# Kernel optimization log

Measured on AMD Instinct MI355X. Metric: run time of the kernel, lower is better.

The kernel has to match this reference:

```python
import jax, jax.numpy as jnp
import numpy as np

B, S, XDIM, YDIM = 64, 1024, 256, 128


def setup_inputs() -> dict:
    key = jax.random.key(0)
    ks = jax.random.split(key, 7)
    q = jax.random.normal(ks[0], (B, S, XDIM), dtype=jnp.float32)
    # Linear weights in torch layout [out, in]; biases [out]
    sc = 1.0 / np.sqrt(XDIM)
    Wq = jax.random.normal(ks[1], (YDIM, XDIM), dtype=jnp.float32) * sc
    Wk = jax.random.normal(ks[2], (YDIM, XDIM), dtype=jnp.float32) * sc
    Wv = jax.random.normal(ks[3], (YDIM, XDIM), dtype=jnp.float32) * sc
    bq = jax.random.normal(ks[4], (YDIM,), dtype=jnp.float32) * sc
    bk = jax.random.normal(ks[5], (YDIM,), dtype=jnp.float32) * sc
    bv = jax.random.normal(ks[6], (YDIM,), dtype=jnp.float32) * sc
    return {"q": q, "Wq": Wq, "bq": bq, "Wk": Wk, "bk": bk, "Wv": Wv, "bv": bv}


def reference(q, Wq, bq, Wk, bk, Wv, bv):
    # Q, K, V projections: [B, S, YDIM]
    Q = jnp.einsum('bsx,yx->bsy', q, Wq) + bq
    K = jnp.einsum('bsx,yx->bsy', q, Wk) + bk
    V = jnp.einsum('bsx,yx->bsy', q, Wv) + bv
    scale = jnp.float32(np.sqrt(YDIM))
    # scores [B, S_q, S_k]; softmax over the QUERY axis (dim=-2), non-standard
    scores = jnp.einsum('bqd,bkd->bqk', Q, K) / scale
    attn = jax.nn.softmax(scores, axis=-2)
    out = jnp.einsum('bqk,bkd->bqd', attn, V)  # [B, S, YDIM]
    # flat=True: max over dim=-2 -> [B, YDIM]
    return jnp.max(out, axis=-2)
```

## Files before the change

kernel.cpp:

```cpp
#include <hip/hip_runtime.h>

typedef __bf16 bf16;
typedef __attribute__((ext_vector_type(8))) __bf16 bf16x8;
typedef __attribute__((ext_vector_type(4))) __bf16 bf16x4;
typedef __attribute__((ext_vector_type(4))) float  f32x4;

static __device__ __forceinline__ f32x4 mfma16(bf16x8 a, bf16x8 b, f32x4 c) {
  return __builtin_amdgcn_mfma_f32_16x16x32_bf16(a, b, c, 0, 0, 0);
}
static __device__ __forceinline__ float fexp2(float x) {
  return __builtin_amdgcn_exp2f(x);
}
static __device__ __forceinline__ float flog2(float x) {
  return __builtin_amdgcn_logf(x);
}

#define EXP_C1 (1.4426950408889634f / 11.313708498984760f)

typedef const __attribute__((address_space(1))) unsigned int gas_u32;
typedef __attribute__((address_space(3))) unsigned int las_u32;
#define GLDS16(gp, lp) __builtin_amdgcn_global_load_lds((gas_u32*)(gp), (las_u32*)(lp), 16, 0, 0)

#define DMA_FENCE() __asm__ volatile("s_waitcnt vmcnt(0)" ::: "memory")


__global__ __launch_bounds__(256) void k_prep(
    const float* __restrict__ Wq, const float* __restrict__ Wk,
    const float* __restrict__ Wv, bf16* __restrict__ Wc, float* __restrict__ out)
{
  int id = blockIdx.x * 256 + threadIdx.x;
  if (id < 8192) out[id] = -__builtin_inff();
  int proj = id >> 12, r = id & 4095;
  int g = r >> 7, n = r & 127;
  const float* W = proj == 0 ? Wq : proj == 1 ? Wk : Wv;
  const float sc = (proj == 0) ? EXP_C1 : 1.0f;
  const float4* src = (const float4*)(W + n * 256 + g * 8);
  float4 a = src[0], b = src[1];
  bf16x8 o = { (bf16)(a.x * sc), (bf16)(a.y * sc), (bf16)(a.z * sc), (bf16)(a.w * sc),
               (bf16)(b.x * sc), (bf16)(b.y * sc), (bf16)(b.z * sc), (bf16)(b.w * sc) };
  *(bf16x8*)(Wc + (size_t)proj * 32768 + g * 1024 + n * 8) = o;
}

__global__ __launch_bounds__(256, 4) void k_qkv(
    const float* __restrict__ q, const bf16* __restrict__ Wc,
    const float* __restrict__ bq, const float* __restrict__ bk, const float* __restrict__ bv,
    bf16* __restrict__ Qb, bf16* __restrict__ Kb, bf16* __restrict__ VT)
{
  __shared__ bf16 Al[32 * 520];

  const int tid = threadIdx.x, lane = tid & 63, wave = tid >> 6;
  const int ln = lane & 15, quad = lane >> 4;
  const int wc = wave;
  const int m0 = blockIdx.x * 64;

  {
    const float* src = q + (size_t)m0 * 256;
    for (int it = 0; it < 16; ++it) {
      int f = it * 1024 + tid * 4;
      int r = f >> 8, c = f & 255;
      float4 v = *(const float4*)(src + f);
      bf16x4 o = { (bf16)v.x, (bf16)v.y, (bf16)v.z, (bf16)v.w };
      *(bf16x4*)&Al[(c >> 3) * 520 + r * 8 + (c & 7)] = o;
    }
  }
  __syncthreads();

  const int b = m0 >> 10, st = (m0 & 1023) >> 7, s_off = m0 & 64;
  const size_t tbase = ((size_t)b * 8 + st) * 16384;

  for (int p = 0; p < 3; ++p) {
    const bf16* W = Wc + (size_t)p * 32768;
    const float* bias = p == 0 ? bq : p == 1 ? bk : bv;
    if (p < 2) {
      f32x4 acc[2][4] = {};
      for (int kk = 0; kk < 8; ++kk) {
        int g = kk * 4 + quad;
        bf16x8 ax[4], bw[2];
        for (int t = 0; t < 4; ++t)
          ax[t] = *(const bf16x8*)&Al[g * 520 + (t * 16 + ln) * 8];
        for (int t = 0; t < 2; ++t)
          bw[t] = *(const bf16x8*)(W + g * 1024 + (wc * 32 + t * 16 + ln) * 8);
        for (int i = 0; i < 2; ++i)
          for (int j = 0; j < 4; ++j)
            acc[i][j] = mfma16(bw[i], ax[j], acc[i][j]);
      }
      bf16* dst = (p == 0 ? Qb : Kb) + tbase;
      for (int i = 0; i < 2; ++i) {
        float4 b4 = *(const float4*)&bias[wc * 32 + i * 16 + quad * 4];
        if (p == 0) { b4.x *= EXP_C1; b4.y *= EXP_C1; b4.z *= EXP_C1; b4.w *= EXP_C1; }
        int gd = wc * 4 + i * 2 + (quad >> 1);
        int e0 = (quad & 1) * 4;
        for (int j = 0; j < 4; ++j) {
          int s = s_off + j * 16 + ln;
          bf16x4 o = { (bf16)(acc[i][j][0] + b4.x), (bf16)(acc[i][j][1] + b4.y),
                       (bf16)(acc[i][j][2] + b4.z), (bf16)(acc[i][j][3] + b4.w) };
          *(bf16x4*)&dst[(size_t)gd * 1024 + (size_t)s * 8 + e0] = o;
        }
      }
    } else {
      f32x4 acc[4][2] = {};
      for (int kk = 0; kk < 8; ++kk) {
        int g = kk * 4 + quad;
        bf16x8 ax[4], bw[2];
        for (int t = 0; t < 4; ++t)
          ax[t] = *(const bf16x8*)&Al[g * 520 + (t * 16 + ln) * 8];
        for (int t = 0; t < 2; ++t)
          bw[t] = *(const bf16x8*)(W + g * 1024 + (wc * 32 + t * 16 + ln) * 8);
        for (int i = 0; i < 4; ++i)
          for (int j = 0; j < 2; ++j)
            acc[i][j] = mfma16(ax[i], bw[j], acc[i][j]);
      }
      bf16* dst = VT + tbase;
      for (int j = 0; j < 2; ++j) {
        int d = wc * 32 + j * 16 + ln;
        float bb = bias[d];
        for (int i = 0; i < 4; ++i) {
          int s0 = s_off + i * 16 + quad * 4;
          int G  = (s0 >> 5) * 4 + ((s0 & 15) >> 2);
          int e0 = (s0 & 16) >> 2;
          bf16x4 o = { (bf16)(acc[i][j][0] + bb), (bf16)(acc[i][j][1] + bb),
                       (bf16)(acc[i][j][2] + bb), (bf16)(acc[i][j][3] + bb) };
          *(bf16x4*)&dst[(size_t)G * 1024 + (size_t)d * 8 + e0] = o;
        }
      }
    }
  }
}

__global__ __launch_bounds__(256, 2) void k_stats(
    const bf16* __restrict__ Qb, const bf16* __restrict__ Kb, float* __restrict__ nlg)
{
  __shared__ char Qbuf[2][32768];
  const int b = blockIdx.x, kt = blockIdx.y;
  const int tid = threadIdx.x, lane = tid & 63, wave = tid >> 6;
  const int ln = lane & 15, quad = lane >> 4;

  const bf16* ktile = Kb + ((size_t)b * 8 + kt) * 16384;
  bf16x8 ak[2][4];
  for (int i = 0; i < 2; ++i)
    for (int kk = 0; kk < 4; ++kk)
      ak[i][kk] = *(const bf16x8*)(ktile + (kk * 4 + quad) * 1024 + (wave * 32 + i * 16 + ln) * 8);

  const char* qb_b = (const char*)(Qb + (size_t)b * 8 * 16384);
  for (int c = 0; c < 8; ++c)
    GLDS16(qb_b + (wave * 8 + c) * 1024 + lane * 16, &Qbuf[0][(wave * 8 + c) * 1024]);

  f32x4 csum[2] = {};
  for (int qt = 0; qt < 8; ++qt) {
    DMA_FENCE();
    __syncthreads();
    if (qt < 7)
      for (int c = 0; c < 8; ++c)
        GLDS16(qb_b + (size_t)(qt + 1) * 32768 + (wave * 8 + c) * 1024 + lane * 16,
               &Qbuf[(qt + 1) & 1][(wave * 8 + c) * 1024]);
    const char* Ql = Qbuf[qt & 1];
    for (int jq = 0; jq < 8; ++jq) {
      f32x4 s0 = {}, s1 = {};
      __builtin_amdgcn_s_setprio(1);
      for (int kk = 0; kk < 4; ++kk) {
        bf16x8 bqf = *(const bf16x8*)(Ql + ((kk * 4 + quad) * 2 + (jq >> 2)) * 1024
                                         + ((jq * 16 + ln) & 63) * 16);
        s0 = mfma16(ak[0][kk], bqf, s0);
        s1 = mfma16(ak[1][kk], bqf, s1);
      }
      __builtin_amdgcn_s_setprio(0);
      for (int rr = 0; rr < 4; ++rr) {
        csum[0][rr] += fexp2(s0[rr]);
        csum[1][rr] += fexp2(s1[rr]);
      }
    }
  }
  for (int i = 0; i < 2; ++i)
    for (int rr = 0; rr < 4; ++rr) {
      float v = csum[i][rr];
      v += __shfl_xor(v, 1, 64); v += __shfl_xor(v, 2, 64);
      v += __shfl_xor(v, 4, 64); v += __shfl_xor(v, 8, 64);
      csum[i][rr] = v;
    }
  if (ln == 0) {
    float* dst = nlg + (size_t)b * 1024 + kt * 128 + wave * 32 + quad * 4;
    for (int i = 0; i < 2; ++i)
      for (int rr = 0; rr < 4; ++rr)
        dst[i * 16 + rr] = -flog2(csum[i][rr]);
  }
}

__global__ __launch_bounds__(256, 2) void k_attn(
    const bf16* __restrict__ Qb, const bf16* __restrict__ Kb, const bf16* __restrict__ VT,
    const float* __restrict__ nlg, float* __restrict__ out)
{
  __shared__ char buf[2][32768];
  __shared__ float nll[1024];
  __shared__ float redm[4][128];

  const int b = blockIdx.x, qt = blockIdx.y;
  const int tid = threadIdx.x, lane = tid & 63, wave = tid >> 6;
  const int ln = lane & 15, quad = lane >> 4;

  *(float4*)&nll[tid * 4] = *(const float4*)(nlg + (size_t)b * 1024 + tid * 4);

  const bf16* qtile = Qb + ((size_t)b * 8 + qt) * 16384;
  bf16x8 bq_[2][4];
  for (int j = 0; j < 2; ++j)
    for (int kk = 0; kk < 4; ++kk)
      bq_[j][kk] = *(const bf16x8*)(qtile + (kk * 4 + quad) * 1024 + (wave * 32 + j * 16 + ln) * 8);

  const char* kb_b = (const char*)(Kb + (size_t)b * 8 * 16384);
  const char* vt_b = (const char*)(VT + (size_t)b * 8 * 16384);

#define DMA_TILE(t) do {                                                         \
    const char* ksrc = kb_b + (size_t)((t) >> 1) * 32768 + ((t) & 1) * 1024;     \
    const char* vsrc = vt_b + (size_t)((t) >> 1) * 32768 + ((t) & 1) * 16384;    \
    char* d_ = buf[(t) & 1];                                                     \
    for (int c = 0; c < 4; ++c) {                                                \
      int ch = wave * 4 + c;                                                     \
      GLDS16(ksrc + ch * 2048 + lane * 16, d_ + ch * 1024);                      \
      GLDS16(vsrc + (ch >> 1) * 2048 + (ch & 1) * 1024 + lane * 16,              \
             d_ + 16384 + ch * 1024);                                            \
    }                                                                            \
  } while (0)

  f32x4 oacc[2][8] = {};
  DMA_TILE(0);

  for (int t = 0; t < 16; ++t) {
    DMA_FENCE();
    __syncthreads();
    if (t < 15) DMA_TILE(t + 1);
    const char* Kl = buf[t & 1];
    const char* Vl = buf[t & 1] + 16384;

    f32x4 sacc[4][2];
    for (int i = 0; i < 4; ++i) {
      float4 L4 = *(float4*)&nll[t * 64 + i * 16 + quad * 4];
      f32x4 ini = { L4.x, L4.y, L4.z, L4.w };
      sacc[i][0] = ini; sacc[i][1] = ini;
    }
    __builtin_amdgcn_s_setprio(1);
    for (int kk = 0; kk < 4; ++kk) {
      bf16x8 ak[4];
      for (int i = 0; i < 4; ++i)
        ak[i] = *(const bf16x8*)(Kl + (kk * 4 + quad) * 1024 + (i * 16 + ln) * 16);
      for (int i = 0; i < 4; ++i)
        for (int j = 0; j < 2; ++j)
          sacc[i][j] = mfma16(ak[i], bq_[j][kk], sacc[i][j]);
    }
    __builtin_amdgcn_s_setprio(0);
    #pragma unroll
    for (int s = 0; s < 2; ++s) {
      f32x4 lo0 = sacc[2 * s][0], hi0 = sacc[2 * s + 1][0];
      f32x4 lo1 = sacc[2 * s][1], hi1 = sacc[2 * s + 1][1];
      bf16x8 pf0 = bf16x8{
        (bf16)fexp2(lo0[0]), (bf16)fexp2(lo0[1]), (bf16)fexp2(lo0[2]), (bf16)fexp2(lo0[3]),
        (bf16)fexp2(hi0[0]), (bf16)fexp2(hi0[1]), (bf16)fexp2(hi0[2]), (bf16)fexp2(hi0[3]) };
      bf16x8 pf1 = bf16x8{
        (bf16)fexp2(lo1[0]), (bf16)fexp2(lo1[1]), (bf16)fexp2(lo1[2]), (bf16)fexp2(lo1[3]),
        (bf16)fexp2(hi1[0]), (bf16)fexp2(hi1[1]), (bf16)fexp2(hi1[2]), (bf16)fexp2(hi1[3]) };
      #pragma unroll
      for (int j2 = 0; j2 < 8; ++j2) {
        bf16x8 bv_ = *(const bf16x8*)(Vl + ((s * 4 + quad) * 2 + (j2 >> 2)) * 1024
                                         + ((j2 * 16 + ln) & 63) * 16);
        oacc[0][j2] = mfma16(pf0, bv_, oacc[0][j2]);
        oacc[1][j2] = mfma16(pf1, bv_, oacc[1][j2]);
      }
    }
  }
#undef DMA_TILE

  for (int j2 = 0; j2 < 8; ++j2) {
    float m = -3.4e38f;
    for (int j = 0; j < 2; ++j)
      for (int rr = 0; rr < 4; ++rr)
        m = fmaxf(m, oacc[j][j2][rr]);
    m = fmaxf(m, __shfl_xor(m, 16, 64));
    m = fmaxf(m, __shfl_xor(m, 32, 64));
    if (lane < 16) redm[wave][j2 * 16 + ln] = m;
  }
  __syncthreads();
  if (tid < 128) {
    float m = fmaxf(fmaxf(redm[0][tid], redm[1][tid]), fmaxf(redm[2][tid], redm[3][tid]));
    float* addr = out + (size_t)b * 128 + tid;
    if (m >= 0.0f) atomicMax((int*)addr, __float_as_int(m));
    else           atomicMin((unsigned int*)addr, __float_as_uint(m));
  }
}

extern "C" void kernel_launch(void* const* d_in, const int* in_sizes, int n_in,
                              void* d_out, int out_size, void* d_ws, size_t ws_size,
                              hipStream_t stream) {
  const float* q  = (const float*)d_in[0];
  const float* Wq = (const float*)d_in[1];
  const float* bq = (const float*)d_in[2];
  const float* Wk = (const float*)d_in[3];
  const float* bk = (const float*)d_in[4];
  const float* Wv = (const float*)d_in[5];
  const float* bv = (const float*)d_in[6];
  float* out = (float*)d_out;

  char* ws = (char*)d_ws;
  bf16*  Qb    = (bf16*)(ws);
  bf16*  Kb    = (bf16*)(ws + (16u << 20));
  bf16*  VT    = (bf16*)(ws + (32u << 20));
  float* nlg   = (float*)(ws + (48u << 20));
  bf16*  Wc    = (bf16*)(ws + (49u << 20));

  k_prep <<<48,           256, 0, stream>>>(Wq, Wk, Wv, Wc, out);
  k_qkv  <<<dim3(1024),   256, 0, stream>>>(q, Wc, bq, bk, bv, Qb, Kb, VT);
  k_stats<<<dim3(64, 8),  256, 0, stream>>>(Qb, Kb, nlg);
  k_attn <<<dim3(64, 8),  256, 0, stream>>>(Qb, Kb, VT, nlg, out);
}
```

Baseline: 87.39 us.

## Software-pipeline QK of next tile with exp/PV of current tile in attention

Splits the shared K/V double buffer into separate K and V buffers, with K prefetched two tiles ahead and V one tile ahead. Each step computes the QK scores for tile t+1 while doing the exp and PV MFMAs for tile t, ping-ponging two score register sets. The goal is to interleave the exp-heavy VALU work with the MFMA work and hide LDS latency. The extra live score registers may raise pressure under launch_bounds(256,2).

```diff
diff --git a/kernel.cpp b/kernel.cpp
--- a/kernel.cpp
+++ b/kernel.cpp
@@ -21,7 +21,7 @@
 typedef __attribute__((address_space(3))) unsigned int las_u32;
 #define GLDS16(gp, lp) __builtin_amdgcn_global_load_lds((gas_u32*)(gp), (las_u32*)(lp), 16, 0, 0)
 
-#define DMA_FENCE() __asm__ volatile("s_waitcnt vmcnt(0)" ::: "memory")
+#define WAITN0() __asm__ volatile("s_waitcnt vmcnt(0)" ::: "memory")
 
 
 __global__ __launch_bounds__(256) void k_prep(
@@ -147,7 +147,7 @@
 
   f32x4 csum[2] = {};
   for (int qt = 0; qt < 8; ++qt) {
-    DMA_FENCE();
+    WAITN0();
     __syncthreads();
     if (qt < 7)
       for (int c = 0; c < 8; ++c)
@@ -189,7 +189,8 @@
     const bf16* __restrict__ Qb, const bf16* __restrict__ Kb, const bf16* __restrict__ VT,
     const float* __restrict__ nlg, float* __restrict__ out)
 {
-  __shared__ char buf[2][32768];
+  __shared__ char bufK[2][16384];
+  __shared__ char bufV[2][16384];
   __shared__ float nll[1024];
   __shared__ float redm[4][128];
 
@@ -208,64 +209,97 @@
   const char* kb_b = (const char*)(Kb + (size_t)b * 8 * 16384);
   const char* vt_b = (const char*)(VT + (size_t)b * 8 * 16384);
 
-#define DMA_TILE(t) do {                                                         \
+#define K_DMA(t) do {                                                            \
     const char* ksrc = kb_b + (size_t)((t) >> 1) * 32768 + ((t) & 1) * 1024;     \
-    const char* vsrc = vt_b + (size_t)((t) >> 1) * 32768 + ((t) & 1) * 16384;    \
-    char* d_ = buf[(t) & 1];                                                     \
+    char* dk = bufK[(t) & 1];                                                    \
     for (int c = 0; c < 4; ++c) {                                                \
       int ch = wave * 4 + c;                                                     \
-      GLDS16(ksrc + ch * 2048 + lane * 16, d_ + ch * 1024);                      \
+      GLDS16(ksrc + ch * 2048 + lane * 16, dk + ch * 1024);                      \
+    }                                                                            \
+  } while (0)
+#define V_DMA(t) do {                                                            \
+    const char* vsrc = vt_b + (size_t)((t) >> 1) * 32768 + ((t) & 1) * 16384;    \
+    char* dv = bufV[(t) & 1];                                                    \
+    for (int c = 0; c < 4; ++c) {                                                \
+      int ch = wave * 4 + c;                                                     \
       GLDS16(vsrc + (ch >> 1) * 2048 + (ch & 1) * 1024 + lane * 16,              \
-             d_ + 16384 + ch * 1024);                                            \
-    }                                                                            \
+             dv + ch * 1024);                                                    \
+    }                                                                            \
+  } while (0)
+
+#define QK(tt, SN) do {                                                          \
+    const char* Kl = bufK[(tt) & 1];                                             \
+    _Pragma("unroll")                                                            \
+    for (int i = 0; i < 4; ++i) {                                                \
+      float4 L4 = *(float4*)&nll[(tt) * 64 + i * 16 + quad * 4];                 \
+      f32x4 ini = { L4.x, L4.y, L4.z, L4.w };                                    \
+      SN[i][0] = ini; SN[i][1] = ini;                                            \
+    }                                                                            \
+    __builtin_amdgcn_s_setprio(1);                                               \
+    _Pragma("unroll")                                                            \
+    for (int kk = 0; kk < 4; ++kk) {                                             \
+      bf16x8 ak[4];                                                              \
+      _Pragma("unroll")                                                          \
+      for (int i = 0; i < 4; ++i)                                                \
+        ak[i] = *(const bf16x8*)(Kl + (kk * 4 + quad) * 1024 + (i * 16 + ln) * 16); \
+      _Pragma("unroll")                                                          \
+      for (int i = 0; i < 4; ++i) {                                              \
+        SN[i][0] = mfma16(ak[i], bq_[0][kk], SN[i][0]);                          \
+        SN[i][1] = mfma16(ak[i], bq_[1][kk], SN[i][1]);                          \
+      }                                                                          \
+    }                                                                            \
+    __builtin_amdgcn_s_setprio(0);                                               \
+  } while (0)
+
+#define EXPPV(tt, SC) do {                                                       \
+    const char* Vl = bufV[(tt) & 1];                                             \
+    _Pragma("unroll")                                                            \
+    for (int s = 0; s < 2; ++s) {                                                \
+      f32x4 lo0 = SC[2 * s][0], hi0 = SC[2 * s + 1][0];                          \
+      f32x4 lo1 = SC[2 * s][1], hi1 = SC[2 * s + 1][1];                          \
+      bf16x8 pf0 = bf16x8{                                                       \
+        (bf16)fexp2(lo0[0]), (bf16)fexp2(lo0[1]), (bf16)fexp2(lo0[2]), (bf16)fexp2(lo0[3]), \
+        (bf16)fexp2(hi0[0]), (bf16)fexp2(hi0[1]), (bf16)fexp2(hi0[2]), (bf16)fexp2(hi0[3]) }; \
+      bf16x8 pf1 = bf16x8{                                                       \
+        (bf16)fexp2(lo1[0]), (bf16)fexp2(lo1[1]), (bf16)fexp2(lo1[2]), (bf16)fexp2(lo1[3]), \
+        (bf16)fexp2(hi1[0]), (bf16)fexp2(hi1[1]), (bf16)fexp2(hi1[2]), (bf16)fexp2(hi1[3]) }; \
+      _Pragma("unroll")                                                          \
+      for (int j2 = 0; j2 < 8; ++j2) {                                           \
+        bf16x8 bv_ = *(const bf16x8*)(Vl + ((s * 4 + quad) * 2 + (j2 >> 2)) * 1024 \
+                                         + ((j2 * 16 + ln) & 63) * 16);          \
+        oacc[0][j2] = mfma16(pf0, bv_, oacc[0][j2]);                             \
+        oacc[1][j2] = mfma16(pf1, bv_, oacc[1][j2]);                             \
+      }                                                                          \
+    }                                                                            \
+  } while (0)
+
+#define STEP(t, CUR, NXT) do {                                                   \
+    WAITN0();                                                                    \
+    __syncthreads();                                                             \
+    if ((t) < 14) K_DMA((t) + 2);                                                \
+    if ((t) < 15) V_DMA((t) + 1);                                                \
+    if ((t) < 15) QK((t) + 1, NXT);                                              \
+    EXPPV((t), CUR);                                                             \
   } while (0)
 
   f32x4 oacc[2][8] = {};
-  DMA_TILE(0);
-
-  for (int t = 0; t < 16; ++t) {
-    DMA_FENCE();
-    __syncthreads();
-    if (t < 15) DMA_TILE(t + 1);
-    const char* Kl = buf[t & 1];
-    const char* Vl = buf[t & 1] + 16384;
-
-    f32x4 sacc[4][2];
-    for (int i = 0; i < 4; ++i) {
-      float4 L4 = *(float4*)&nll[t * 64 + i * 16 + quad * 4];
-      f32x4 ini = { L4.x, L4.y, L4.z, L4.w };
-      sacc[i][0] = ini; sacc[i][1] = ini;
-    }
-    __builtin_amdgcn_s_setprio(1);
-    for (int kk = 0; kk < 4; ++kk) {
-      bf16x8 ak[4];
-      for (int i = 0; i < 4; ++i)
-        ak[i] = *(const bf16x8*)(Kl + (kk * 4 + quad) * 1024 + (i * 16 + ln) * 16);
-      for (int i = 0; i < 4; ++i)
-        for (int j = 0; j < 2; ++j)
-          sacc[i][j] = mfma16(ak[i], bq_[j][kk], sacc[i][j]);
-    }
-    __builtin_amdgcn_s_setprio(0);
-    #pragma unroll
-    for (int s = 0; s < 2; ++s) {
-      f32x4 lo0 = sacc[2 * s][0], hi0 = sacc[2 * s + 1][0];
-      f32x4 lo1 = sacc[2 * s][1], hi1 = sacc[2 * s + 1][1];
-      bf16x8 pf0 = bf16x8{
-        (bf16)fexp2(lo0[0]), (bf16)fexp2(lo0[1]), (bf16)fexp2(lo0[2]), (bf16)fexp2(lo0[3]),
-        (bf16)fexp2(hi0[0]), (bf16)fexp2(hi0[1]), (bf16)fexp2(hi0[2]), (bf16)fexp2(hi0[3]) };
-      bf16x8 pf1 = bf16x8{
-        (bf16)fexp2(lo1[0]), (bf16)fexp2(lo1[1]), (bf16)fexp2(lo1[2]), (bf16)fexp2(lo1[3]),
-        (bf16)fexp2(hi1[0]), (bf16)fexp2(hi1[1]), (bf16)fexp2(hi1[2]), (bf16)fexp2(hi1[3]) };
-      #pragma unroll
-      for (int j2 = 0; j2 < 8; ++j2) {
-        bf16x8 bv_ = *(const bf16x8*)(Vl + ((s * 4 + quad) * 2 + (j2 >> 2)) * 1024
-                                         + ((j2 * 16 + ln) & 63) * 16);
-        oacc[0][j2] = mfma16(pf0, bv_, oacc[0][j2]);
-        oacc[1][j2] = mfma16(pf1, bv_, oacc[1][j2]);
-      }
-    }
-  }
-#undef DMA_TILE
+  f32x4 sA[4][2], sB[4][2];
+
+  K_DMA(0);
+  WAITN0();
+  __syncthreads();
+  K_DMA(1); V_DMA(0);
+  QK(0, sA);
+
+  for (int tp = 0; tp < 8; ++tp) {
+    STEP(2 * tp,     sA, sB);
+    STEP(2 * tp + 1, sB, sA);
+  }
+#undef STEP
+#undef EXPPV
+#undef QK
+#undef K_DMA
+#undef V_DMA
 
   for (int j2 = 0; j2 < 8; ++j2) {
     float m = -3.4e38f;
```

After: 86.73 us. No clear change (-0.8%).
